# Kernel tuning notes

Hardware: AMD Instinct MI355X
Metric: run time of the kernel (lower is better)

The kernel has to match this reference:

```python
import jax, jax.numpy as jnp
import numpy as np

N_NODES = 100000
N_EDGES = 6400000
D_FEAT = 128

def setup_inputs() -> dict:
    key = jax.random.key(0)
    k1, k2, k3 = jax.random.split(key, 3)
    h = jax.random.normal(k1, (N_NODES, D_FEAT), dtype=jnp.float32)
    src = jax.random.randint(k2, (N_EDGES,), 0, N_NODES, dtype=jnp.int64)
    dst = jax.random.randint(k3, (N_EDGES,), 0, N_NODES, dtype=jnp.int64)
    return {"h": h, "src": src, "dst": dst}

def reference(h, src, dst):
    N = h.shape[0]
    pos = h[:, 0]                                  # [N] scalar position per node
    # per-edge message: |pos_src - pos_dst|
    dist = jnp.abs(pos[src] - pos[dst])            # [E]
    # segment-mean over incoming edges at each dst node
    s = jax.ops.segment_sum(dist, dst, num_segments=N)                  # [N]
    cnt = jax.ops.segment_sum(jnp.ones_like(dist), dst, num_segments=N)  # [N] in-degree
    h_dst = s / jnp.maximum(cnt, 1.0)              # zero-in-degree nodes -> 0 (DGL default)
    return jnp.stack([pos, h_dst], axis=1)         # [N, 2]
```

## Files before the change

### kernel.cpp

```cpp
#include <hip/hip_runtime.h>
#include <hip/hip_fp16.h>

#define D_FEAT 128
#define NBINS_MAX 10
#define BIN_SIZE 10000
#define PB 2000
#define PB_THREADS 256
#define CAP 512
#define CAP_SHIFT 9
#define LBSTRIDE (CAP + 4)
#define SBB 25
#define SEGS (PB / SBB)
#define SC_THREADS 1024
#define DIST_SCALE 1024.0f
#define INV_DIST_SCALE (1.0f / 1024.0f)

__global__ void init_pos(const float* __restrict__ h, float* __restrict__ pos,
                         unsigned short* __restrict__ posh, int n) {
    int i = blockIdx.x * blockDim.x + threadIdx.x;
    if (i < n) {
        float v = h[(size_t)i * D_FEAT];
        pos[i] = v;
        posh[i] = __half_as_ushort(__float2half(v));
    }
}

__global__ __launch_bounds__(PB_THREADS, 8) void prep_kernel(
        const int* __restrict__ src, const int* __restrict__ dst,
        unsigned int* __restrict__ pv2, unsigned int* __restrict__ cnts,
        int n_edges, int nbins, int chunk) {
    __shared__ unsigned int cursor[NBINS_MAX];
    __shared__ __align__(16) unsigned int lbin[NBINS_MAX * LBSTRIDE];
    const int b = blockIdx.x;
    const int t = threadIdx.x;
    if (t < nbins) cursor[t] = 0u;
    __syncthreads();

    const long base = (long)b * chunk;
    long lim = (long)n_edges - base;
    if (lim > chunk) lim = chunk;
    if (lim < 0) lim = 0;

#define PREP_ONE(dd, ss)                                                        \
    {                                                                           \
        unsigned int d = (unsigned int)(dd);                                    \
        unsigned int bin = d / BIN_SIZE;                                        \
        unsigned int drel = d - bin * BIN_SIZE;                                 \
        unsigned int slot = atomicAdd(&cursor[bin], 1u);                        \
        if (slot < CAP)                                                         \
            lbin[bin * LBSTRIDE + slot] = ((unsigned int)(ss) << 14) | drel;    \
    }

    const long R = (lim / (PB_THREADS * 12)) * (PB_THREADS * 12);
    for (long k0 = (long)t * 12; k0 < R; k0 += PB_THREADS * 12) {
        const int* dp = dst + base + k0;
        const int* sp = src + base + k0;
        int4 da = *(const int4*)dp;
        int4 db = *(const int4*)(dp + 4);
        int4 dc = *(const int4*)(dp + 8);
        int4 sa = *(const int4*)sp;
        int4 sb = *(const int4*)(sp + 4);
        int4 sc = *(const int4*)(sp + 8);
        PREP_ONE(da.x, sa.x);
        PREP_ONE(da.y, sa.y);
        PREP_ONE(da.z, sa.z);
        PREP_ONE(da.w, sa.w);
        PREP_ONE(db.x, sb.x);
        PREP_ONE(db.y, sb.y);
        PREP_ONE(db.z, sb.z);
        PREP_ONE(db.w, sb.w);
        PREP_ONE(dc.x, sc.x);
        PREP_ONE(dc.y, sc.y);
        PREP_ONE(dc.z, sc.z);
        PREP_ONE(dc.w, sc.w);
    }
    for (long k = R + t; k < lim; k += PB_THREADS) {
        PREP_ONE(dst[base + k], src[base + k]);
    }
#undef PREP_ONE
    __syncthreads();

    for (int bin = 0; bin < nbins; ++bin) {
        int cnt = (int)min(cursor[bin], (unsigned int)CAP);
        unsigned int* op = pv2 + (((size_t)bin * PB + b) << CAP_SHIFT);
        for (int w = t * 4; w < cnt; w += PB_THREADS * 4)
            *(uint4*)(op + w) = *(const uint4*)&lbin[bin * LBSTRIDE + w];
    }
    if (t < nbins) cnts[t * PB + b] = min(cursor[t], (unsigned int)CAP);
}

__global__ __launch_bounds__(SC_THREADS) void scatter_kernel(
        const unsigned int* __restrict__ pv2, const unsigned int* __restrict__ cnts,
        const float* __restrict__ pos, const unsigned short* __restrict__ posh,
        unsigned int* __restrict__ part, int n_nodes) {
    __shared__ unsigned int lacc[BIN_SIZE];
    __shared__ float pos_lds[BIN_SIZE];
    __shared__ unsigned int cl[SEGS];
    const int bx = blockIdx.x;
    const int bin = bx / SBB;
    const int j = bx - bin * SBB;
    const int bin_lo = bin * BIN_SIZE;
    const int bin_n = min(BIN_SIZE, n_nodes - bin_lo);
    const int t = threadIdx.x;

    if (t < SEGS) cl[t] = cnts[bin * PB + j * SEGS + t];
    for (int k = t; k < bin_n; k += SC_THREADS) {
        lacc[k] = 0u;
        pos_lds[k] = pos[bin_lo + k];
    }
    __syncthreads();

#define SC_BODY(vv, hh)                                                         \
    {                                                                           \
        float a = __half2float(__ushort_as_half((unsigned short)(hh)));         \
        unsigned int r = (vv) & 0x3FFFu;                                        \
        unsigned int f = min((unsigned int)(fabsf(a - pos_lds[r]) * DIST_SCALE + 0.5f), 16383u); \
        atomicAdd(&lacc[r], (1u << 24) | f);                                    \
    }

    const unsigned int* pj = pv2 + (((size_t)bin * PB + (size_t)j * SEGS) << CAP_SHIFT);
    const int TOT = SEGS * CAP;
    for (int idx = t * 8; idx < TOT; idx += SC_THREADS * 8) {
        int seg = idx >> CAP_SHIFT;
        int slot = idx & (CAP - 1);
        int cnt = (int)cl[seg];
        const unsigned int* p = pj + ((size_t)seg << CAP_SHIFT);
        if (slot + 8 <= cnt) {
            uint4 va = *(const uint4*)(p + slot);
            uint4 vb = *(const uint4*)(p + slot + 4);
            unsigned short h0 = posh[va.x >> 14];
            unsigned short h1 = posh[va.y >> 14];
            unsigned short h2 = posh[va.z >> 14];
            unsigned short h3 = posh[va.w >> 14];
            unsigned short h4 = posh[vb.x >> 14];
            unsigned short h5 = posh[vb.y >> 14];
            unsigned short h6 = posh[vb.z >> 14];
            unsigned short h7 = posh[vb.w >> 14];
            SC_BODY(va.x, h0); SC_BODY(va.y, h1); SC_BODY(va.z, h2); SC_BODY(va.w, h3);
            SC_BODY(vb.x, h4); SC_BODY(vb.y, h5); SC_BODY(vb.z, h6); SC_BODY(vb.w, h7);
        } else if (slot < cnt) {
            for (int q = slot; q < cnt && q < slot + 8; ++q) {
                unsigned int v = p[q];
                SC_BODY(v, posh[v >> 14]);
            }
        }
    }
#undef SC_BODY
    __syncthreads();

    unsigned int* slice = part + (size_t)j * n_nodes + bin_lo;
    for (int k = t; k < bin_n; k += SC_THREADS) slice[k] = lacc[k];
}

__global__ void merge_kernel(const float* __restrict__ pos,
                             const unsigned int* __restrict__ part,
                             float* __restrict__ out, int n_nodes) {
    int i0 = (blockIdx.x * blockDim.x + threadIdx.x) * 4;
    if (i0 + 4 <= n_nodes) {
        unsigned int c0 = 0, c1 = 0, c2 = 0, c3 = 0;
        unsigned int s0 = 0, s1 = 0, s2 = 0, s3 = 0;
        for (int b = 0; b < SBB; ++b) {
            uint4 p = *(const uint4*)(part + (size_t)b * n_nodes + i0);
            c0 += p.x >> 24; s0 += p.x & 0x00FFFFFFu;
            c1 += p.y >> 24; s1 += p.y & 0x00FFFFFFu;
            c2 += p.z >> 24; s2 += p.z & 0x00FFFFFFu;
            c3 += p.w >> 24; s3 += p.w & 0x00FFFFFFu;
        }
        float4 ps = *(const float4*)(pos + i0);
        float4 oa, ob;
        oa.x = ps.x; oa.y = ((float)s0 * INV_DIST_SCALE) / fmaxf((float)c0, 1.0f);
        oa.z = ps.y; oa.w = ((float)s1 * INV_DIST_SCALE) / fmaxf((float)c1, 1.0f);
        ob.x = ps.z; ob.y = ((float)s2 * INV_DIST_SCALE) / fmaxf((float)c2, 1.0f);
        ob.z = ps.w; ob.w = ((float)s3 * INV_DIST_SCALE) / fmaxf((float)c3, 1.0f);
        ((float4*)out)[(i0 >> 1)] = oa;
        ((float4*)out)[(i0 >> 1) + 1] = ob;
    } else {
        for (int i = i0; i < n_nodes; ++i) {
            unsigned int cnt = 0, sum = 0;
            for (int b = 0; b < SBB; ++b) {
                unsigned int p = part[(size_t)b * n_nodes + i];
                cnt += p >> 24;
                sum += p & 0x00FFFFFFu;
            }
            float2 o;
            o.x = pos[i];
            o.y = ((float)sum * INV_DIST_SCALE) / fmaxf((float)cnt, 1.0f);
            ((float2*)out)[i] = o;
        }
    }
}

__global__ void fb_init(const float* __restrict__ h, float* __restrict__ pos,
                        unsigned long long* __restrict__ acc, int n) {
    int i = blockIdx.x * blockDim.x + threadIdx.x;
    if (i < n) { pos[i] = h[(size_t)i * D_FEAT]; acc[i] = 0ull; }
}
__global__ void fb_edge(const int* __restrict__ src, const int* __restrict__ dst,
                        const float* __restrict__ pos,
                        unsigned long long* __restrict__ acc, int n_edges) {
    int stride = gridDim.x * blockDim.x;
    for (int i = blockIdx.x * blockDim.x + threadIdx.x; i < n_edges; i += stride) {
        float dist = fabsf(pos[src[i]] - pos[dst[i]]);
        unsigned int fx = (unsigned int)(dist * 262144.0f + 0.5f);
        atomicAdd(&acc[dst[i]], (1ull << 32) | (unsigned long long)fx);
    }
}
__global__ void fb_final(const float* __restrict__ pos,
                         const unsigned long long* __restrict__ acc,
                         float* __restrict__ out, int n) {
    int i = blockIdx.x * blockDim.x + threadIdx.x;
    if (i < n) {
        unsigned long long v = acc[i];
        unsigned int cnt = (unsigned int)(v >> 32);
        float s = (float)(unsigned int)(v & 0xffffffffull) * (1.0f / 262144.0f);
        float2 o; o.x = pos[i]; o.y = s / fmaxf((float)cnt, 1.0f);
        ((float2*)out)[i] = o;
    }
}

extern "C" void kernel_launch(void* const* d_in, const int* in_sizes, int n_in,
                              void* d_out, int out_size, void* d_ws, size_t ws_size,
                              hipStream_t stream) {
    const float* h = (const float*)d_in[0];
    const int* src = (const int*)d_in[1];
    const int* dst = (const int*)d_in[2];
    float* out = (float*)d_out;

    int n_nodes = in_sizes[0] / D_FEAT;
    int n_edges = in_sizes[1];

    int chunk = (n_edges + PB - 1) / PB;
    int nbins = (n_nodes + BIN_SIZE - 1) / BIN_SIZE;
    size_t pos_bytes  = ((size_t)n_nodes * 4 + 255) & ~(size_t)255;
    size_t posh_bytes = ((size_t)n_nodes * 2 + 255) & ~(size_t)255;
    size_t pv2_bytes  = (((size_t)nbins * PB << CAP_SHIFT) * 4 + 255) & ~(size_t)255;
    size_t cnts_bytes = ((size_t)nbins * PB * 4 + 255) & ~(size_t)255;
    size_t part_bytes = (size_t)SBB * n_nodes * 4;
    bool fast_ok = (ws_size >= pos_bytes + posh_bytes + pv2_bytes + cnts_bytes + part_bytes) &&
                   (n_nodes <= (1 << 17)) && (nbins <= NBINS_MAX) &&
                   ((size_t)chunk * 10 <= (size_t)CAP * nbins * 7);

    int block = 256;
    int ngrid = (n_nodes + block - 1) / block;

    if (fast_ok) {
        char* w = (char*)d_ws;
        float* pos = (float*)w;                          w += pos_bytes;
        unsigned short* posh = (unsigned short*)w;       w += posh_bytes;
        unsigned int* pv2 = (unsigned int*)w;            w += pv2_bytes;
        unsigned int* cnts = (unsigned int*)w;           w += cnts_bytes;
        unsigned int* part = (unsigned int*)w;
        init_pos<<<ngrid, block, 0, stream>>>(h, pos, posh, n_nodes);
        prep_kernel<<<PB, PB_THREADS, 0, stream>>>(src, dst, pv2, cnts,
                                                   n_edges, nbins, chunk);
        scatter_kernel<<<nbins * SBB, SC_THREADS, 0, stream>>>(pv2, cnts, pos, posh,
                                                               part, n_nodes);
        int mgrid = (n_nodes + block * 4 - 1) / (block * 4);
        merge_kernel<<<mgrid, block, 0, stream>>>(pos, part, out, n_nodes);
    } else {
        float* pos = (float*)d_ws;
        unsigned long long* acc = (unsigned long long*)((char*)d_ws + pos_bytes);
        fb_init<<<ngrid, block, 0, stream>>>(h, pos, acc, n_nodes);
        fb_edge<<<(n_edges + block - 1) / block, block, 0, stream>>>(src, dst, pos, acc, n_edges);
        fb_final<<<ngrid, block, 0, stream>>>(pos, acc, out, n_nodes);
    }
}
```

Before: 165.9 us.

## Halve bin size, atomically merge per-slice scatter results into one accumulator

Bin size drops to 5000 nodes with 20 bins, and per-bin capacity is halved to 256. The scatter kernel now atomically adds its nonzero LDS counters straight into a single global accumulator instead of writing 25 partial slices. The merge kernel therefore reads one value per node rather than summing 25 slices. In prep, each wave copies out a separate bin. Smaller LDS per scatter block should allow more resident blocks, at the cost of twice as many scatter blocks and global atomics. The packed 8-bit count and 24-bit sum fields are now summed across all slices in one word, so overflow headroom shrinks.

```diff
diff --git a/kernel.cpp b/kernel.cpp
--- a/kernel.cpp
+++ b/kernel.cpp
@@ -2,12 +2,12 @@
 #include <hip/hip_fp16.h>
 
 #define D_FEAT 128
-#define NBINS_MAX 10
-#define BIN_SIZE 10000
+#define NBINS_MAX 20
+#define BIN_SIZE 5000
 #define PB 2000
 #define PB_THREADS 256
-#define CAP 512
-#define CAP_SHIFT 9
+#define CAP 256
+#define CAP_SHIFT 8
 #define LBSTRIDE (CAP + 4)
 #define SBB 25
 #define SEGS (PB / SBB)
@@ -16,12 +16,14 @@
 #define INV_DIST_SCALE (1.0f / 1024.0f)
 
 __global__ void init_pos(const float* __restrict__ h, float* __restrict__ pos,
-                         unsigned short* __restrict__ posh, int n) {
+                         unsigned short* __restrict__ posh,
+                         unsigned int* __restrict__ acc, int n) {
     int i = blockIdx.x * blockDim.x + threadIdx.x;
     if (i < n) {
         float v = h[(size_t)i * D_FEAT];
         pos[i] = v;
         posh[i] = __half_as_ushort(__float2half(v));
+        acc[i] = 0u;
     }
 }
 
@@ -80,11 +82,15 @@
 #undef PREP_ONE
     __syncthreads();
 
-    for (int bin = 0; bin < nbins; ++bin) {
-        int cnt = (int)min(cursor[bin], (unsigned int)CAP);
-        unsigned int* op = pv2 + (((size_t)bin * PB + b) << CAP_SHIFT);
-        for (int w = t * 4; w < cnt; w += PB_THREADS * 4)
-            *(uint4*)(op + w) = *(const uint4*)&lbin[bin * LBSTRIDE + w];
+    {
+        const int wave = t >> 6;
+        const int lane = t & 63;
+        for (int bin = wave; bin < nbins; bin += (PB_THREADS >> 6)) {
+            int cnt = (int)min(cursor[bin], (unsigned int)CAP);
+            unsigned int* op = pv2 + (((size_t)bin * PB + b) << CAP_SHIFT);
+            for (int w = lane * 4; w < cnt; w += 64 * 4)
+                *(uint4*)(op + w) = *(const uint4*)&lbin[bin * LBSTRIDE + w];
+        }
     }
     if (t < nbins) cnts[t * PB + b] = min(cursor[t], (unsigned int)CAP);
 }
@@ -92,7 +98,7 @@
 __global__ __launch_bounds__(SC_THREADS) void scatter_kernel(
         const unsigned int* __restrict__ pv2, const unsigned int* __restrict__ cnts,
         const float* __restrict__ pos, const unsigned short* __restrict__ posh,
-        unsigned int* __restrict__ part, int n_nodes) {
+        unsigned int* __restrict__ acc, int n_nodes) {
     __shared__ unsigned int lacc[BIN_SIZE];
     __shared__ float pos_lds[BIN_SIZE];
     __shared__ unsigned int cl[SEGS];
@@ -148,43 +154,32 @@
 #undef SC_BODY
     __syncthreads();
 
-    unsigned int* slice = part + (size_t)j * n_nodes + bin_lo;
-    for (int k = t; k < bin_n; k += SC_THREADS) slice[k] = lacc[k];
-}
-
-__global__ void merge_kernel(const float* __restrict__ pos,
-                             const unsigned int* __restrict__ part,
-                             float* __restrict__ out, int n_nodes) {
+    for (int k = t; k < bin_n; k += SC_THREADS) {
+        unsigned int v = lacc[k];
+        if (v) atomicAdd(&acc[bin_lo + k], v);
+    }
+}
+
+__global__ void out_kernel(const float* __restrict__ pos,
+                           const unsigned int* __restrict__ acc,
+                           float* __restrict__ out, int n_nodes) {
     int i0 = (blockIdx.x * blockDim.x + threadIdx.x) * 4;
     if (i0 + 4 <= n_nodes) {
-        unsigned int c0 = 0, c1 = 0, c2 = 0, c3 = 0;
-        unsigned int s0 = 0, s1 = 0, s2 = 0, s3 = 0;
-        for (int b = 0; b < SBB; ++b) {
-            uint4 p = *(const uint4*)(part + (size_t)b * n_nodes + i0);
-            c0 += p.x >> 24; s0 += p.x & 0x00FFFFFFu;
-            c1 += p.y >> 24; s1 += p.y & 0x00FFFFFFu;
-            c2 += p.z >> 24; s2 += p.z & 0x00FFFFFFu;
-            c3 += p.w >> 24; s3 += p.w & 0x00FFFFFFu;
-        }
+        uint4 a = *(const uint4*)(acc + i0);
         float4 ps = *(const float4*)(pos + i0);
         float4 oa, ob;
-        oa.x = ps.x; oa.y = ((float)s0 * INV_DIST_SCALE) / fmaxf((float)c0, 1.0f);
-        oa.z = ps.y; oa.w = ((float)s1 * INV_DIST_SCALE) / fmaxf((float)c1, 1.0f);
-        ob.x = ps.z; ob.y = ((float)s2 * INV_DIST_SCALE) / fmaxf((float)c2, 1.0f);
-        ob.z = ps.w; ob.w = ((float)s3 * INV_DIST_SCALE) / fmaxf((float)c3, 1.0f);
+        oa.x = ps.x; oa.y = ((float)(a.x & 0x00FFFFFFu) * INV_DIST_SCALE) / fmaxf((float)(a.x >> 24), 1.0f);
+        oa.z = ps.y; oa.w = ((float)(a.y & 0x00FFFFFFu) * INV_DIST_SCALE) / fmaxf((float)(a.y >> 24), 1.0f);
+        ob.x = ps.z; ob.y = ((float)(a.z & 0x00FFFFFFu) * INV_DIST_SCALE) / fmaxf((float)(a.z >> 24), 1.0f);
+        ob.z = ps.w; ob.w = ((float)(a.w & 0x00FFFFFFu) * INV_DIST_SCALE) / fmaxf((float)(a.w >> 24), 1.0f);
         ((float4*)out)[(i0 >> 1)] = oa;
         ((float4*)out)[(i0 >> 1) + 1] = ob;
     } else {
         for (int i = i0; i < n_nodes; ++i) {
-            unsigned int cnt = 0, sum = 0;
-            for (int b = 0; b < SBB; ++b) {
-                unsigned int p = part[(size_t)b * n_nodes + i];
-                cnt += p >> 24;
-                sum += p & 0x00FFFFFFu;
-            }
+            unsigned int a = acc[i];
             float2 o;
             o.x = pos[i];
-            o.y = ((float)sum * INV_DIST_SCALE) / fmaxf((float)cnt, 1.0f);
+            o.y = ((float)(a & 0x00FFFFFFu) * INV_DIST_SCALE) / fmaxf((float)(a >> 24), 1.0f);
             ((float2*)out)[i] = o;
         }
     }
@@ -235,8 +230,8 @@
     size_t posh_bytes = ((size_t)n_nodes * 2 + 255) & ~(size_t)255;
     size_t pv2_bytes  = (((size_t)nbins * PB << CAP_SHIFT) * 4 + 255) & ~(size_t)255;
     size_t cnts_bytes = ((size_t)nbins * PB * 4 + 255) & ~(size_t)255;
-    size_t part_bytes = (size_t)SBB * n_nodes * 4;
-    bool fast_ok = (ws_size >= pos_bytes + posh_bytes + pv2_bytes + cnts_bytes + part_bytes) &&
+    size_t acc_bytes  = ((size_t)n_nodes * 4 + 255) & ~(size_t)255;
+    bool fast_ok = (ws_size >= pos_bytes + posh_bytes + pv2_bytes + cnts_bytes + acc_bytes) &&
                    (n_nodes <= (1 << 17)) && (nbins <= NBINS_MAX) &&
                    ((size_t)chunk * 10 <= (size_t)CAP * nbins * 7);
 
@@ -249,14 +244,14 @@
         unsigned short* posh = (unsigned short*)w;       w += posh_bytes;
         unsigned int* pv2 = (unsigned int*)w;            w += pv2_bytes;
         unsigned int* cnts = (unsigned int*)w;           w += cnts_bytes;
-        unsigned int* part = (unsigned int*)w;
-        init_pos<<<ngrid, block, 0, stream>>>(h, pos, posh, n_nodes);
+        unsigned int* acc = (unsigned int*)w;
+        init_pos<<<ngrid, block, 0, stream>>>(h, pos, posh, acc, n_nodes);
         prep_kernel<<<PB, PB_THREADS, 0, stream>>>(src, dst, pv2, cnts,
                                                    n_edges, nbins, chunk);
         scatter_kernel<<<nbins * SBB, SC_THREADS, 0, stream>>>(pv2, cnts, pos, posh,
-                                                               part, n_nodes);
-        int mgrid = (n_nodes + block * 4 - 1) / (block * 4);
-        merge_kernel<<<mgrid, block, 0, stream>>>(pos, part, out, n_nodes);
+                                                               acc, n_nodes);
+        int ogrid = (n_nodes + block * 4 - 1) / (block * 4);
+        out_kernel<<<ogrid, block, 0, stream>>>(pos, acc, out, n_nodes);
     } else {
         float* pos = (float*)d_ws;
         unsigned long long* acc = (unsigned long long*)((char*)d_ws + pos_bytes);
```

Result: faster. 160.2 us (-3.5%).
